# Optimization experiments

Measured on AMD Instinct MI355X. Metric: run time of the kernel, lower is better.

Reference implementation:

```python
import jax, jax.numpy as jnp
from jax import lax
import numpy as np

B, T = 128, 28
N = T - 1  # 27 recurrent steps


def conv(x, w, b, stride=1, pad=1):
    y = lax.conv_general_dilated(x, w, (stride, stride), [(pad, pad), (pad, pad)],
                                 dimension_numbers=('NCHW', 'OIHW', 'NCHW'))
    return y + b[None, :, None, None]


def convT(x, w, b, stride, pad, out_pad):
    # torch ConvTranspose2d: weight layout [in, out, k, k]
    k = w.shape[-1]
    wt = jnp.flip(w, (-2, -1)).transpose(1, 0, 2, 3)  # -> [out, in, k, k]
    lo, hi = k - 1 - pad, k - 1 - pad + out_pad
    y = lax.conv_general_dilated(x, wt, (1, 1), [(lo, hi), (lo, hi)],
                                 lhs_dilation=(stride, stride),
                                 dimension_numbers=('NCHW', 'OIHW', 'NCHW'))
    return y + b[None, :, None, None]


def setup_inputs():
    key = jax.random.key(0)
    ki = iter(jax.random.split(key, 48))
    def cw(o, i, k=3):
        return jax.random.normal(next(ki), (o, i, k, k), jnp.float32) / np.sqrt(i * k * k)
    def bias(o):
        return jax.random.normal(next(ki), (o,), jnp.float32) * 0.02
    H, I = 16 * 8 * 8, 48 * 8 * 8
    return {
        'x': jax.random.uniform(next(ki), (B, T, 3, 32, 32), jnp.float32),
        'eps': jax.random.normal(next(ki), (N, B, 64, 8, 8), jnp.float32),
        'psix1_w': cw(16, 3),  'psix1_b': bias(16),
        'psix2_w': cw(16, 16), 'psix2_b': bias(16),
        'psiz_w': cw(16, 64),  'psiz_b': bias(16),
        'enc1_w': cw(32, 32),  'enc1_b': bias(32),
        'enc2_w': cw(64, 32),  'enc2_b': bias(64),
        'encm_w': cw(64, 64),  'encm_b': bias(64),
        'encv_w': cw(64, 64),  'encv_b': bias(64),
        'pri_w': cw(32, 16),   'pri_b': bias(32),
        'prim_w': cw(64, 32),  'prim_b': bias(64),
        'priv_w': cw(64, 32),  'priv_b': bias(64),
        'dec1_w': jax.random.normal(next(ki), (32, 32, 3, 3), jnp.float32) / np.sqrt(32 * 9),
        'dec1_b': bias(32),
        'dec2_w': jax.random.normal(next(ki), (32, 3, 3, 3), jnp.float32) / np.sqrt(32 * 9),
        'dec2_b': bias(3),
        'gru_wi': jax.random.normal(next(ki), (3 * H, I), jnp.float32) / np.sqrt(I),
        'gru_wh': jax.random.normal(next(ki), (3 * H, H), jnp.float32) / np.sqrt(H),
        'gru_bi': bias(3 * H),
        'gru_bh': bias(3 * H),
    }


def _forward(x, eps, psix1_w, psix1_b, psix2_w, psix2_b, psiz_w, psiz_b,
             enc1_w, enc1_b, enc2_w, enc2_b, encm_w, encm_b, encv_w, encv_b,
             pri_w, pri_b, prim_w, prim_b, priv_w, priv_b,
             dec1_w, dec1_b, dec2_w, dec2_b, gru_wi, gru_wh, gru_bi, gru_bh):
    Bn = x.shape[0]
    Hf = 16 * 8 * 8
    n = x.shape[1] - 1

    def step(carry, inputs):
        h0, dec_prev, _, _, _, _ = carry
        frame, ep, idx = inputs
        cur = jnp.where(idx < 6, frame, dec_prev)
        px = jax.nn.relu(conv(cur, psix1_w, psix1_b, 2, 1))   # [B,16,16,16]
        px = jax.nn.relu(conv(px, psix2_w, psix2_b, 2, 1))    # [B,16,8,8]
        e = jnp.concatenate([px, h0], axis=1)                 # [B,32,8,8]
        e = jax.nn.relu(conv(e, enc1_w, enc1_b))
        e = jax.nn.relu(conv(e, enc2_w, enc2_b))              # [B,64,8,8]
        zm = conv(e, encm_w, encm_b)
        zlv = jax.nn.softplus(conv(e, encv_w, encv_b))
        p = jax.nn.relu(conv(h0, pri_w, pri_b))               # [B,32,8,8]
        pm = conv(p, prim_w, prim_b)
        plv = jax.nn.softplus(conv(p, priv_w, priv_b))
        z = zm + zlv * ep                                     # source's literal reparam (uses logvar, not std)
        zpsi = jax.nn.relu(conv(z, psiz_w, psiz_b))           # [B,16,8,8]
        d = jnp.concatenate([h0, zpsi], axis=1)               # [B,32,8,8]
        d = jax.nn.relu(convT(d, dec1_w, dec1_b, 2, 1, 0))    # 8 -> 15
        dec = jax.nn.sigmoid(convT(d, dec2_w, dec2_b, 2, 0, 1))  # 15 -> 32, [B,3,32,32]
        # GRUCell on flattened concat
        gi = jnp.concatenate([px, zpsi, h0], axis=1).reshape(Bn, -1)  # [B, 48*8*8]
        hf = h0.reshape(Bn, Hf)
        gih = gi @ gru_wi.T + gru_bi
        ghh = hf @ gru_wh.T + gru_bh
        ir, iz, inn = jnp.split(gih, 3, axis=1)
        hr, hz, hn = jnp.split(ghh, 3, axis=1)
        r = jax.nn.sigmoid(ir + hr)
        u = jax.nn.sigmoid(iz + hz)
        ng = jnp.tanh(inn + r * hn)
        hnew = ((1.0 - u) * ng + u * hf).reshape(Bn, 16, 8, 8)
        return (hnew, dec, zm, zlv, pm, plv), dec

    h0 = jnp.zeros((Bn, 16, 8, 8), jnp.float32)
    dec0 = jnp.zeros((Bn, 3, 32, 32), jnp.float32)
    s0 = jnp.zeros((Bn, 64, 8, 8), jnp.float32)
    frames = jnp.swapaxes(x[:, :n], 0, 1)  # [N,B,3,32,32]
    (_, _, zm, zlv, pm, plv), decs = lax.scan(
        step, (h0, dec0, s0, s0, s0, s0), (frames, eps, jnp.arange(n)))
    output = jnp.swapaxes(decs, 0, 1)  # [B,N,3,32,32]
    return output, zm, zlv, pm, plv


def reference(x, eps, psix1_w, psix1_b, psix2_w, psix2_b, psiz_w, psiz_b,
              enc1_w, enc1_b, enc2_w, enc2_b, encm_w, encm_b, encv_w, encv_b,
              pri_w, pri_b, prim_w, prim_b, priv_w, priv_b,
              dec1_w, dec1_b, dec2_w, dec2_b, gru_wi, gru_wh, gru_bi, gru_bh):
    return _forward(x, eps, psix1_w, psix1_b, psix2_w, psix2_b, psiz_w, psiz_b,
                    enc1_w, enc1_b, enc2_w, enc2_b, encm_w, encm_b, encv_w, encv_b,
                    pri_w, pri_b, prim_w, prim_b, priv_w, priv_b,
                    dec1_w, dec1_b, dec2_w, dec2_b, gru_wi, gru_wh, gru_bi, gru_bh)
```

## Files before the change

kernel.cpp:

```cpp
#include <hip/hip_runtime.h>

#define NSTEP 27

typedef _Float16 f16;
typedef __attribute__((ext_vector_type(8))) _Float16 f16x8;
typedef __attribute__((ext_vector_type(4))) float f32x4;

#define MFMA(a, b, c) __builtin_amdgcn_mfma_f32_16x16x32_f16(a, b, c, 0, 0, 0)

__device__ __forceinline__ float sigmoidf_(float x) { return 1.0f / (1.0f + expf(-x)); }
__device__ __forceinline__ float softplusf_(float x) { return x > 20.0f ? x : log1pf(expf(x)); }

constexpr long OFF_WI   = 0;
constexpr long OFF_WH   = OFF_WI   + 3072L * 3072;
constexpr long OFF_WPX1 = OFF_WH   + 3072L * 1024;
constexpr long OFF_WPX2 = OFF_WPX1 + 512;
constexpr long OFF_WE1  = OFF_WPX2 + 2560;
constexpr long OFF_WE2  = OFF_WE1  + 9216;
constexpr long OFF_WMV  = OFF_WE2  + 18432;
constexpr long OFF_WPZ  = OFF_WMV  + 73728;
constexpr long OFF_WPRI = OFF_WPZ  + 9216;
constexpr long OFF_WPMV = OFF_WPRI + 5120;
constexpr long OFF_WD1  = OFF_WPMV + 36864;
constexpr long OFF_GI   = OFF_WD1  + 9216;
constexpr long OFF_F16_END = OFF_GI + 128L * 3072;

struct Params {
  const float* frame; long fstride;
  const float* eps_t;
  const f16 *wpx1, *wpx2, *we1, *we2, *wmv, *wpz, *wd1, *wpri, *wpmv;
  const float *bpx1, *bpx2, *be1, *be2, *bm, *bv, *bpz, *bd1;
  const float *d2w, *d2b, *bpri, *bpm, *bpv, *gbi, *gbh;
  const float *gih0, *gih1, *ghh;
  float* hG; f16* gi;
  float *out_t, *zm, *zlv, *pm, *plv;
  int t, last;
};

__device__ __forceinline__ void scat8_lds(f16* __restrict__ A, int ldk, int pos, int ic, float val) {
  int py = pos >> 3, px = pos & 7;
  f16 v = (f16)val;
#pragma unroll
  for (int ky = 0; ky < 3; ++ky) {
    int oy = py + 1 - ky;
    if ((unsigned)oy >= 8u) continue;
#pragma unroll
    for (int kx = 0; kx < 3; ++kx) {
      int ox = px + 1 - kx;
      if ((unsigned)ox >= 8u) continue;
      A[(oy * 8 + ox) * ldk + ic * 9 + ky * 3 + kx] = v;
    }
  }
}

__device__ __forceinline__ void scatd1_lds(f16* __restrict__ Ad1, int pos, int ic, float val) {
  const int aof[4] = {0, 2560, 7168, 11776};
  const int Kp[4] = {40, 72, 72, 136};
  int py = pos >> 3, px = pos & 7;
  f16 v = (f16)val;
#pragma unroll
  for (int ky = 0; ky < 3; ++ky) {
    int y = 2 * py + ky - 1;
    if ((unsigned)y >= 15u) continue;
    int cy = y & 1;
    int nky = cy ? 2 : 1;
    int tiy = cy ? (ky >> 1) : 0;
#pragma unroll
    for (int kx = 0; kx < 3; ++kx) {
      int x = 2 * px + kx - 1;
      if ((unsigned)x >= 15u) continue;
      int cx = x & 1;
      int nkx = cx ? 2 : 1;
      int tix = cx ? (kx >> 1) : 0;
      int c = cy * 2 + cx;
      Ad1[aof[c] + ((y >> 1) * 8 + (x >> 1)) * Kp[c] + ic * (nky * nkx) + tiy * nkx + tix] = v;
    }
  }
}

__global__ __launch_bounds__(256) void k_wpack(const float* __restrict__ src, f16* __restrict__ dst,
                                               int N, int Ks, int Kd) {
  int tot = N * Kd, stride = gridDim.x * 256;
  for (int i = blockIdx.x * 256 + threadIdx.x; i < tot; i += stride) {
    int n = i / Kd, k = i - n * Kd;
    dst[i] = (k < Ks) ? (f16)src[n * Ks + k] : (f16)0.f;
  }
}

__global__ __launch_bounds__(256) void k_wd1(const float* __restrict__ src, f16* __restrict__ dst) {
  int i = blockIdx.x * 256 + threadIdx.x;
  if (i >= 9216) return;
  int c, base;
  if (i < 1024) { c = 0; base = 0; }
  else if (i < 3072) { c = 1; base = 1024; }
  else if (i < 5120) { c = 2; base = 3072; }
  else { c = 3; base = 5120; }
  const int Kc[4] = {32, 64, 64, 128};
  int j = i - base, K = Kc[c];
  int oc = j / K, k = j - oc * K;
  int cy = c >> 1, cx = c & 1;
  int nky = cy ? 2 : 1, nkx = cx ? 2 : 1, ntap = nky * nkx;
  int ic = k / ntap, tap = k - ic * ntap;
  int tiy = tap / nkx, tix = tap - tiy * nkx;
  int ky = (nky == 1) ? 1 : tiy * 2;
  int kx = (nkx == 1) ? 1 : tix * 2;
  dst[i] = (f16)src[((ic * 32 + oc) * 3 + ky) * 3 + kx];
}

__global__ __launch_bounds__(512) void k_step(Params P) {
  __shared__ f16 lds[78336];
  f16* hbuf = lds;
  f16* B1 = lds + 1024;
  f16* B2 = lds + 38400;
  f16* B3 = lds + 57344;
  f16* A1 = B3;
  f16* frame = B3 + 10240;
  f16* A2 = B3 + 10240;

  int b = blockIdx.x, tid = threadIdx.x;
  int wv = tid >> 6, lane = tid & 63, lm = lane & 15, q = lane >> 4;
  f32x4 z4 = {};

  for (int i = tid; i < 1024; i += 512) {
    float hn = 0.f;
    if (P.t) {
      long o = (long)b * 3072 + i;
      float ir  = P.gih0[o] + P.gih1[o] + P.gbi[i];
      float iz  = P.gih0[o + 1024] + P.gih1[o + 1024] + P.gbi[i + 1024];
      float in_ = P.gih0[o + 2048] + P.gih1[o + 2048] + P.gbi[i + 2048];
      float hr  = P.ghh[o] + P.gbh[i];
      float hz  = P.ghh[o + 1024] + P.gbh[i + 1024];
      float hnn = P.ghh[o + 2048] + P.gbh[i + 2048];
      float r = sigmoidf_(ir + hr), u = sigmoidf_(iz + hz);
      float ng = tanhf(in_ + r * hnn);
      hn = (1.f - u) * ng + u * P.hG[b * 1024 + i];
    }
    P.hG[b * 1024 + i] = hn;
    hbuf[i] = (f16)hn;
    P.gi[(long)b * 3072 + 2048 + i] = (f16)hn;
  }
  const float* fr = P.frame + (long)b * P.fstride;
  for (int i = tid; i < 3072; i += 512) frame[i] = (f16)fr[i];
  __syncthreads();
  {
    int row = tid >> 1, half = tid & 1;
    int oy = row >> 4, ox = row & 15;
    f16* rp = A1 + row * 40;
    if (half == 0) {
#pragma unroll
      for (int ic = 0; ic < 2; ++ic)
#pragma unroll
        for (int ky = 0; ky < 3; ++ky) {
          int y = 2 * oy + ky - 1;
#pragma unroll
          for (int kx = 0; kx < 3; ++kx) {
            int x = 2 * ox + kx - 1;
            rp[ic * 9 + ky * 3 + kx] =
                ((unsigned)y < 32u && (unsigned)x < 32u) ? frame[ic * 1024 + y * 32 + x] : (f16)0;
          }
        }
    } else {
#pragma unroll
      for (int ky = 0; ky < 3; ++ky) {
        int y = 2 * oy + ky - 1;
#pragma unroll
        for (int kx = 0; kx < 3; ++kx) {
          int x = 2 * ox + kx - 1;
          rp[18 + ky * 3 + kx] =
              ((unsigned)y < 32u && (unsigned)x < 32u) ? frame[2048 + y * 32 + x] : (f16)0;
        }
      }
#pragma unroll
      for (int k = 27; k < 40; ++k) rp[k] = (f16)0;
    }
  }
  __syncthreads();
  {
    int4 zz = {0, 0, 0, 0};
    for (int i = tid; i < 10752 / 8; i += 512) ((int4*)A2)[i] = zz;
    for (int i = tid; i < 18944 / 8; i += 512) ((int4*)B2)[i] = zz;
    for (int i = tid; i < 37376 / 8; i += 512) ((int4*)B1)[i] = zz;
  }
  __syncthreads();
  for (int i = tid; i < 1024; i += 512)
    scat8_lds(B2, 296, i & 63, 16 + (i >> 6), (float)hbuf[i]);
  {
    f16x8 bf = *(const f16x8*)(P.wpx1 + lm * 32 + q * 8);
    float bb = P.bpx1[lm];
#pragma unroll
    for (int mi = 0; mi < 2; ++mi) {
      int mt = wv * 2 + mi;
      f16x8 a = *(const f16x8*)(A1 + (mt * 16 + lm) * 40 + q * 8);
      f32x4 acc = MFMA(a, bf, z4);
#pragma unroll
      for (int r = 0; r < 4; ++r) {
        int m = mt * 16 + q * 4 + r;
        float val = fmaxf(acc[r] + bb, 0.f);
        int y = m >> 4, x = m & 15;
        f16 v = (f16)val;
#pragma unroll
        for (int ky = 0; ky < 3; ++ky) {
          int ty = y + 1 - ky;
          if (ty < 0 || (ty & 1)) continue;
          int oy = ty >> 1; if (oy >= 8) continue;
#pragma unroll
          for (int kx = 0; kx < 3; ++kx) {
            int tx = x + 1 - kx;
            if (tx < 0 || (tx & 1)) continue;
            int ox = tx >> 1; if (ox >= 8) continue;
            A2[(oy * 8 + ox) * 168 + lm * 9 + ky * 3 + kx] = v;
          }
        }
      }
    }
  }
  __syncthreads();
  if (wv < 4) {
    f32x4 acc = {};
#pragma unroll
    for (int k = 0; k < 160; k += 32) {
      f16x8 a = *(const f16x8*)(A2 + (wv * 16 + lm) * 168 + k + q * 8);
      f16x8 bf = *(const f16x8*)(P.wpx2 + lm * 160 + k + q * 8);
      acc = MFMA(a, bf, acc);
    }
    float bb = P.bpx2[lm];
#pragma unroll
    for (int r = 0; r < 4; ++r) {
      int pos = wv * 16 + q * 4 + r;
      float val = fmaxf(acc[r] + bb, 0.f);
      P.gi[(long)b * 3072 + lm * 64 + pos] = (f16)val;
      scat8_lds(B2, 296, pos, lm, val);
    }
  }
  __syncthreads();
  {
    int nt = wv & 1, mt = wv >> 1;
    f32x4 a0 = {};
#pragma unroll
    for (int k = 0; k < 288; k += 32) {
      f16x8 bf = *(const f16x8*)(P.we1 + (nt * 16 + lm) * 288 + k + q * 8);
      f16x8 x0 = *(const f16x8*)(B2 + (mt * 16 + lm) * 296 + k + q * 8);
      a0 = MFMA(x0, bf, a0);
    }
    for (int i = tid; i < 1024; i += 512)
      scatd1_lds(B3, i & 63, i >> 6, (float)hbuf[i]);
    __syncthreads();
    float bb = P.be1[nt * 16 + lm];
#pragma unroll
    for (int r = 0; r < 4; ++r)
      scat8_lds(B2, 296, mt * 16 + q * 4 + r, nt * 16 + lm, fmaxf(a0[r] + bb, 0.f));
  }
  __syncthreads();
  {
    int nt = wv & 3, mh = wv >> 2;
    f32x4 acc[2] = {};
#pragma unroll
    for (int k = 0; k < 288; k += 32) {
      f16x8 bf = *(const f16x8*)(P.we2 + (nt * 16 + lm) * 288 + k + q * 8);
#pragma unroll
      for (int mi = 0; mi < 2; ++mi) {
        f16x8 a = *(const f16x8*)(B2 + ((mh * 2 + mi) * 16 + lm) * 296 + k + q * 8);
        acc[mi] = MFMA(a, bf, acc[mi]);
      }
    }
    int ch = nt * 16 + lm;
    float bb = P.be2[ch];
#pragma unroll
    for (int mi = 0; mi < 2; ++mi)
#pragma unroll
      for (int r = 0; r < 4; ++r)
        scat8_lds(B1, 584, (mh * 2 + mi) * 16 + q * 4 + r, ch, fmaxf(acc[mi][r] + bb, 0.f));
  }
  __syncthreads();
  {
    f32x4 am[2] = {}, av[2] = {};
    int nq = wv & 3, mh = wv >> 2;
    int ch = nq * 16 + lm;
#pragma unroll 2
    for (int k = 0; k < 576; k += 32) {
      f16x8 bm = *(const f16x8*)(P.wmv + (long)ch * 576 + k + q * 8);
      f16x8 bv = *(const f16x8*)(P.wmv + (long)(64 + ch) * 576 + k + q * 8);
#pragma unroll
      for (int mi = 0; mi < 2; ++mi) {
        f16x8 a = *(const f16x8*)(B1 + ((mh * 2 + mi) * 16 + lm) * 584 + k + q * 8);
        am[mi] = MFMA(a, bm, am[mi]);
        av[mi] = MFMA(a, bv, av[mi]);
      }
    }
    __syncthreads();
    float bbm = P.bm[ch], bbv = P.bv[ch];
#pragma unroll
    for (int mi = 0; mi < 2; ++mi)
#pragma unroll
      for (int r = 0; r < 4; ++r) {
        int pos = (mh * 2 + mi) * 16 + q * 4 + r;
        float zmv = am[mi][r] + bbm;
        float sp = softplusf_(av[mi][r] + bbv);
        float zval = zmv + sp * P.eps_t[(long)b * 4096 + ch * 64 + pos];
        if (P.last) {
          P.zm[(long)b * 4096 + ch * 64 + pos] = zmv;
          P.zlv[(long)b * 4096 + ch * 64 + pos] = sp;
        }
        scat8_lds(B1, 584, pos, ch, zval);
      }
  }
  __syncthreads();
  if (wv < 4) {
    f32x4 acc = {};
#pragma unroll 2
    for (int k = 0; k < 576; k += 32) {
      f16x8 a = *(const f16x8*)(B1 + (wv * 16 + lm) * 584 + k + q * 8);
      f16x8 bf = *(const f16x8*)(P.wpz + (long)lm * 576 + k + q * 8);
      acc = MFMA(a, bf, acc);
    }
    float bb = P.bpz[lm];
#pragma unroll
    for (int r = 0; r < 4; ++r) {
      int pos = wv * 16 + q * 4 + r;
      float val = fmaxf(acc[r] + bb, 0.f);
      P.gi[(long)b * 3072 + 1024 + lm * 64 + pos] = (f16)val;
      scatd1_lds(B3, pos, 16 + lm, val);
    }
  }
  __syncthreads();
  {
    const int Kc[4] = {32, 64, 64, 128};
    const int Kp[4] = {40, 72, 72, 136};
    const int aof[4] = {0, 2560, 7168, 11776};
    const int bof[4] = {0, 1024, 3072, 5120};
    int nt = wv & 1, mt = wv >> 1;
#pragma unroll
    for (int c = 0; c < 4; ++c) {
      int cy = c >> 1, cx = c & 1;
      f32x4 acc = {};
      for (int k = 0; k < Kc[c]; k += 32) {
        f16x8 a = *(const f16x8*)(B3 + aof[c] + (mt * 16 + lm) * Kp[c] + k + q * 8);
        f16x8 bf = *(const f16x8*)(P.wd1 + bof[c] + (nt * 16 + lm) * Kc[c] + k + q * 8);
        acc = MFMA(a, bf, acc);
      }
      int oc = nt * 16 + lm;
      float bb = P.bd1[oc];
#pragma unroll
      for (int r = 0; r < 4; ++r) {
        int m = mt * 16 + q * 4 + r;
        int y = 2 * (m >> 3) + cy, x = 2 * (m & 7) + cx;
        if (y < 15 && x < 15)
          B2[oc * 240 + y * 15 + x] = (f16)fmaxf(acc[r] + bb, 0.f);
      }
    }
  }
  __syncthreads();
  {
    int p = wv & 3, jh = wv >> 2;
    int cy2 = p >> 1, cx2 = p & 1;
    int lx = lane & 15, ly = lane >> 4;
    int x = 2 * lx + cx2;
    float b0 = P.d2b[0], b1 = P.d2b[1], b2 = P.d2b[2];
    float acc[2][3];
#pragma unroll
    for (int j = 0; j < 2; ++j) { acc[j][0] = b0; acc[j][1] = b1; acc[j][2] = b2; }
    int nky = cy2 ? 1 : 2, nkx = cx2 ? 1 : 2;
    for (int ic = 0; ic < 32; ++ic) {
      const f16* sp = B2 + ic * 240;
      const float* wic = P.d2w + ic * 27;
      for (int ty = 0; ty < nky; ++ty) {
        int ky = cy2 ? 1 : ty * 2;
        for (int tx = 0; tx < nkx; ++tx) {
          int kx = cx2 ? 1 : tx * 2;
          int ix = (x - kx) >> 1;
          bool xv = (unsigned)ix < 15u;
          float w0 = wic[ky * 3 + kx];
          float w1 = wic[9 + ky * 3 + kx];
          float w2 = wic[18 + ky * 3 + kx];
#pragma unroll
          for (int j = 0; j < 2; ++j) {
            int py = (jh * 2 + j) * 4 + ly;
            int iy = (2 * py + cy2 - ky) >> 1;
            if (xv && (unsigned)iy < 15u) {
              float v = (float)sp[iy * 15 + ix];
              acc[j][0] += v * w0; acc[j][1] += v * w1; acc[j][2] += v * w2;
            }
          }
        }
      }
    }
#pragma unroll
    for (int j = 0; j < 2; ++j) {
      int y = 2 * ((jh * 2 + j) * 4 + ly) + cy2;
#pragma unroll
      for (int oc = 0; oc < 3; ++oc)
        P.out_t[(long)b * 82944 + oc * 1024 + y * 32 + x] = sigmoidf_(acc[j][oc]);
    }
  }
  if (P.last) {
    if (tid < 64) {
      int py = tid >> 3, px = tid & 7;
      f16* rp = B3 + tid * 168;
      int k = 0;
      for (int ic = 0; ic < 16; ++ic)
        for (int ky = 0; ky < 3; ++ky) {
          int y = py + ky - 1;
          for (int kx = 0; kx < 3; ++kx, ++k) {
            int x = px + kx - 1;
            rp[k] = ((unsigned)y < 8u && (unsigned)x < 8u) ? hbuf[ic * 64 + y * 8 + x] : (f16)0;
          }
        }
      for (; k < 168; ++k) rp[k] = (f16)0;
    }
    {
      int4 zz = {0, 0, 0, 0};
      for (int i = tid; i < 18944 / 8; i += 512) ((int4*)B1)[i] = zz;
    }
    __syncthreads();
    {
      int nt = wv & 1, mt = wv >> 1;
      f32x4 a0 = {};
#pragma unroll
      for (int k = 0; k < 160; k += 32) {
        f16x8 bf = *(const f16x8*)(P.wpri + (nt * 16 + lm) * 160 + k + q * 8);
        f16x8 x0 = *(const f16x8*)(B3 + (mt * 16 + lm) * 168 + k + q * 8);
        a0 = MFMA(x0, bf, a0);
      }
      float bb = P.bpri[nt * 16 + lm];
#pragma unroll
      for (int r = 0; r < 4; ++r)
        scat8_lds(B1, 296, mt * 16 + q * 4 + r, nt * 16 + lm, fmaxf(a0[r] + bb, 0.f));
    }
    __syncthreads();
    {
      f32x4 am[2] = {}, av[2] = {};
      int nq = wv & 3, mh = wv >> 2;
      int ch = nq * 16 + lm;
#pragma unroll
      for (int k = 0; k < 288; k += 32) {
        f16x8 bm = *(const f16x8*)(P.wpmv + (long)ch * 288 + k + q * 8);
        f16x8 bv = *(const f16x8*)(P.wpmv + (long)(64 + ch) * 288 + k + q * 8);
#pragma unroll
        for (int mi = 0; mi < 2; ++mi) {
          f16x8 a = *(const f16x8*)(B1 + ((mh * 2 + mi) * 16 + lm) * 296 + k + q * 8);
          am[mi] = MFMA(a, bm, am[mi]);
          av[mi] = MFMA(a, bv, av[mi]);
        }
      }
      float bbm = P.bpm[ch], bbv = P.bpv[ch];
#pragma unroll
      for (int mi = 0; mi < 2; ++mi)
#pragma unroll
        for (int r = 0; r < 4; ++r) {
          int pos = (mh * 2 + mi) * 16 + q * 4 + r;
          P.pm[(long)b * 4096 + ch * 64 + pos] = am[mi][r] + bbm;
          P.plv[(long)b * 4096 + ch * 64 + pos] = softplusf_(av[mi][r] + bbv);
        }
    }
  }
}

__global__ __launch_bounds__(128) void k_gru(const f16* __restrict__ gi,
                                             const f16* __restrict__ wi, const f16* __restrict__ wh,
                                             float* __restrict__ gih0, float* __restrict__ gih1,
                                             float* __restrict__ ghh) {
  int z = blockIdx.y;
  int wv = threadIdx.x >> 6, lane = threadIdx.x & 63, lm = lane & 15, q = lane >> 4;
  int gw = blockIdx.x * 2 + wv;
  int mg = gw & 1, ng = gw >> 1;
  const f16* A = (z == 2) ? gi + 2048 : gi;
  const f16* B = (z == 2) ? wh : wi;
  int K = (z == 2) ? 1024 : 1536;
  int k0 = (z == 1) ? 1536 : 0;
  long ldb = (z == 2) ? 1024 : 3072;
  float* out = (z == 0) ? gih0 : (z == 1) ? gih1 : ghh;
  int m0 = mg * 64, n0 = ng * 32;
  f32x4 acc[4][2] = {};
  const f16* Ap = A + (long)(m0 + lm) * 3072 + k0 + q * 8;
  const f16* Bp = B + (long)(n0 + lm) * ldb + k0 + q * 8;
#pragma unroll 2
  for (int k = 0; k < K; k += 32) {
    f16x8 b0 = *(const f16x8*)(Bp + k);
    f16x8 b1 = *(const f16x8*)(Bp + 16 * ldb + k);
#pragma unroll
    for (int i = 0; i < 4; ++i) {
      f16x8 a = *(const f16x8*)(Ap + (long)i * 16 * 3072 + k);
      acc[i][0] = MFMA(a, b0, acc[i][0]);
      acc[i][1] = MFMA(a, b1, acc[i][1]);
    }
  }
#pragma unroll
  for (int i = 0; i < 4; ++i)
#pragma unroll
    for (int j = 0; j < 2; ++j)
#pragma unroll
      for (int r = 0; r < 4; ++r)
        out[(long)(m0 + i * 16 + q * 4 + r) * 3072 + n0 + j * 16 + lm] = acc[i][j][r];
}

extern "C" void kernel_launch(void* const* d_in, const int* in_sizes, int n_in,
                              void* d_out, int out_size, void* d_ws, size_t ws_size,
                              hipStream_t stream) {
  const float* x       = (const float*)d_in[0];
  const float* eps     = (const float*)d_in[1];
  const float* psix1_w = (const float*)d_in[2];
  const float* psix1_b = (const float*)d_in[3];
  const float* psix2_w = (const float*)d_in[4];
  const float* psix2_b = (const float*)d_in[5];
  const float* psiz_w  = (const float*)d_in[6];
  const float* psiz_b  = (const float*)d_in[7];
  const float* enc1_w  = (const float*)d_in[8];
  const float* enc1_b  = (const float*)d_in[9];
  const float* enc2_w  = (const float*)d_in[10];
  const float* enc2_b  = (const float*)d_in[11];
  const float* encm_w  = (const float*)d_in[12];
  const float* encm_b  = (const float*)d_in[13];
  const float* encv_w  = (const float*)d_in[14];
  const float* encv_b  = (const float*)d_in[15];
  const float* pri_w   = (const float*)d_in[16];
  const float* pri_b   = (const float*)d_in[17];
  const float* prim_w  = (const float*)d_in[18];
  const float* prim_b  = (const float*)d_in[19];
  const float* priv_w  = (const float*)d_in[20];
  const float* priv_b  = (const float*)d_in[21];
  const float* dec1_w  = (const float*)d_in[22];
  const float* dec1_b  = (const float*)d_in[23];
  const float* dec2_w  = (const float*)d_in[24];
  const float* dec2_b  = (const float*)d_in[25];
  const float* gru_wi  = (const float*)d_in[26];
  const float* gru_wh  = (const float*)d_in[27];
  const float* gru_bi  = (const float*)d_in[28];
  const float* gru_bh  = (const float*)d_in[29];

  float* out = (float*)d_out;
  float* zm_out  = out + 10616832;
  float* zlv_out = zm_out + 524288;
  float* pm_out  = zlv_out + 524288;
  float* plv_out = pm_out + 524288;

  f16* ws16 = (f16*)d_ws;
  f16* wi_f  = ws16 + OFF_WI;
  f16* wh_f  = ws16 + OFF_WH;
  f16* w_px1 = ws16 + OFF_WPX1;
  f16* w_px2 = ws16 + OFF_WPX2;
  f16* w_e1  = ws16 + OFF_WE1;
  f16* w_e2  = ws16 + OFF_WE2;
  f16* w_mv  = ws16 + OFF_WMV;
  f16* w_pz  = ws16 + OFF_WPZ;
  f16* w_pri = ws16 + OFF_WPRI;
  f16* w_pmv = ws16 + OFF_WPMV;
  f16* w_d1  = ws16 + OFF_WD1;
  f16* gi    = ws16 + OFF_GI;
  float* fws = (float*)(ws16 + OFF_F16_END);
  float* gih0 = fws;
  float* gih1 = gih0 + 393216;
  float* ghh  = gih1 + 393216;
  float* hG   = ghh + 393216;

  k_wpack<<<2048, 256, 0, stream>>>(gru_wi, wi_f, 3072, 3072, 3072);
  k_wpack<<<1024, 256, 0, stream>>>(gru_wh, wh_f, 3072, 1024, 1024);
  k_wpack<<<2, 256, 0, stream>>>(psix1_w, w_px1, 16, 27, 32);
  k_wpack<<<10, 256, 0, stream>>>(psix2_w, w_px2, 16, 144, 160);
  k_wpack<<<36, 256, 0, stream>>>(enc1_w, w_e1, 32, 288, 288);
  k_wpack<<<72, 256, 0, stream>>>(enc2_w, w_e2, 64, 288, 288);
  k_wpack<<<144, 256, 0, stream>>>(encm_w, w_mv, 64, 576, 576);
  k_wpack<<<144, 256, 0, stream>>>(encv_w, w_mv + 64L * 576, 64, 576, 576);
  k_wpack<<<36, 256, 0, stream>>>(psiz_w, w_pz, 16, 576, 576);
  k_wpack<<<20, 256, 0, stream>>>(pri_w, w_pri, 32, 144, 160);
  k_wpack<<<72, 256, 0, stream>>>(prim_w, w_pmv, 64, 288, 288);
  k_wpack<<<72, 256, 0, stream>>>(priv_w, w_pmv + 64L * 288, 64, 288, 288);
  k_wd1<<<36, 256, 0, stream>>>(dec1_w, w_d1);

  for (int t = 0; t < NSTEP; ++t) {
    Params P;
    P.frame = (t < 6) ? x + (long)t * 3072 : out + (long)(t - 1) * 3072;
    P.fstride = (t < 6) ? 86016 : 82944;
    P.eps_t = eps + (long)t * 524288;
    P.wpx1 = w_px1; P.wpx2 = w_px2; P.we1 = w_e1; P.we2 = w_e2;
    P.wmv = w_mv; P.wpz = w_pz; P.wd1 = w_d1; P.wpri = w_pri; P.wpmv = w_pmv;
    P.bpx1 = psix1_b; P.bpx2 = psix2_b; P.be1 = enc1_b; P.be2 = enc2_b;
    P.bm = encm_b; P.bv = encv_b; P.bpz = psiz_b; P.bd1 = dec1_b;
    P.d2w = dec2_w; P.d2b = dec2_b; P.bpri = pri_b; P.bpm = prim_b; P.bpv = priv_b;
    P.gbi = gru_bi; P.gbh = gru_bh;
    P.gih0 = gih0; P.gih1 = gih1; P.ghh = ghh;
    P.hG = hG; P.gi = gi;
    P.out_t = out + (long)t * 3072;
    P.zm = zm_out; P.zlv = zlv_out; P.pm = pm_out; P.plv = plv_out;
    P.t = t; P.last = (t == NSTEP - 1);
    k_step<<<128, 512, 0, stream>>>(P);
    if (t < NSTEP - 1)
      k_gru<<<dim3(96, 3), 128, 0, stream>>>(gi, wi_f, wh_f, gih0, gih1, ghh);
  }
}
```

Before: 2.736 ms.

## Double k_step block to 1024 threads and split per-wave work across 16 waves

Launches the per-sample step kernel with 1024 threads instead of 512 and redistributes each conv stage so every wave handles one M tile instead of two. The zeroing of LDS buffers is overlapped with im2col construction, and the transposed-conv decoder phases are split across more waves. This targets latency in a kernel with only 128 blocks by exposing more parallelism per block. The cost is higher register pressure under the 1024-thread launch bound and idle waves in stages that only use 4 or 8 waves.

```diff
diff --git a/kernel.cpp b/kernel.cpp
--- a/kernel.cpp
+++ b/kernel.cpp
@@ -107,7 +107,7 @@
   dst[i] = (f16)src[((ic * 32 + oc) * 3 + ky) * 3 + kx];
 }
 
-__global__ __launch_bounds__(512) void k_step(Params P) {
+__global__ __launch_bounds__(1024) void k_step(Params P) {
   __shared__ f16 lds[78336];
   f16* hbuf = lds;
   f16* B1 = lds + 1024;
@@ -121,7 +121,8 @@
   int wv = tid >> 6, lane = tid & 63, lm = lane & 15, q = lane >> 4;
   f32x4 z4 = {};
 
-  for (int i = tid; i < 1024; i += 512) {
+  {
+    int i = tid;
     float hn = 0.f;
     if (P.t) {
       long o = (long)b * 3072 + i;
@@ -140,9 +141,9 @@
     P.gi[(long)b * 3072 + 2048 + i] = (f16)hn;
   }
   const float* fr = P.frame + (long)b * P.fstride;
-  for (int i = tid; i < 3072; i += 512) frame[i] = (f16)fr[i];
-  __syncthreads();
-  {
+  for (int i = tid; i < 3072; i += 1024) frame[i] = (f16)fr[i];
+  __syncthreads();
+  if (tid < 512) {
     int row = tid >> 1, half = tid & 1;
     int oy = row >> 4, ox = row & 15;
     f16* rp = A1 + row * 40;
@@ -173,43 +174,42 @@
 #pragma unroll
       for (int k = 27; k < 40; ++k) rp[k] = (f16)0;
     }
-  }
-  __syncthreads();
-  {
+  } else {
     int4 zz = {0, 0, 0, 0};
-    for (int i = tid; i < 10752 / 8; i += 512) ((int4*)A2)[i] = zz;
-    for (int i = tid; i < 18944 / 8; i += 512) ((int4*)B2)[i] = zz;
-    for (int i = tid; i < 37376 / 8; i += 512) ((int4*)B1)[i] = zz;
-  }
-  __syncthreads();
-  for (int i = tid; i < 1024; i += 512)
-    scat8_lds(B2, 296, i & 63, 16 + (i >> 6), (float)hbuf[i]);
+    int t2 = tid - 512;
+    for (int i = t2; i < 18944 / 8; i += 512) ((int4*)B2)[i] = zz;
+    for (int i = t2; i < 37376 / 8; i += 512) ((int4*)B1)[i] = zz;
+  }
+  __syncthreads();
+  {
+    int4 zz = {0, 0, 0, 0};
+    for (int i = tid; i < 10752 / 8; i += 1024) ((int4*)A2)[i] = zz;
+  }
+  __syncthreads();
+  scat8_lds(B2, 296, tid & 63, 16 + (tid >> 6), (float)hbuf[tid]);
   {
     f16x8 bf = *(const f16x8*)(P.wpx1 + lm * 32 + q * 8);
     float bb = P.bpx1[lm];
-#pragma unroll
-    for (int mi = 0; mi < 2; ++mi) {
-      int mt = wv * 2 + mi;
-      f16x8 a = *(const f16x8*)(A1 + (mt * 16 + lm) * 40 + q * 8);
-      f32x4 acc = MFMA(a, bf, z4);
-#pragma unroll
-      for (int r = 0; r < 4; ++r) {
-        int m = mt * 16 + q * 4 + r;
-        float val = fmaxf(acc[r] + bb, 0.f);
-        int y = m >> 4, x = m & 15;
-        f16 v = (f16)val;
-#pragma unroll
-        for (int ky = 0; ky < 3; ++ky) {
-          int ty = y + 1 - ky;
-          if (ty < 0 || (ty & 1)) continue;
-          int oy = ty >> 1; if (oy >= 8) continue;
-#pragma unroll
-          for (int kx = 0; kx < 3; ++kx) {
-            int tx = x + 1 - kx;
-            if (tx < 0 || (tx & 1)) continue;
-            int ox = tx >> 1; if (ox >= 8) continue;
-            A2[(oy * 8 + ox) * 168 + lm * 9 + ky * 3 + kx] = v;
-          }
+    int mt = wv;
+    f16x8 a = *(const f16x8*)(A1 + (mt * 16 + lm) * 40 + q * 8);
+    f32x4 acc = MFMA(a, bf, z4);
+#pragma unroll
+    for (int r = 0; r < 4; ++r) {
+      int m = mt * 16 + q * 4 + r;
+      float val = fmaxf(acc[r] + bb, 0.f);
+      int y = m >> 4, x = m & 15;
+      f16 v = (f16)val;
+#pragma unroll
+      for (int ky = 0; ky < 3; ++ky) {
+        int ty = y + 1 - ky;
+        if (ty < 0 || (ty & 1)) continue;
+        int oy = ty >> 1; if (oy >= 8) continue;
+#pragma unroll
+        for (int kx = 0; kx < 3; ++kx) {
+          int tx = x + 1 - kx;
+          if (tx < 0 || (tx & 1)) continue;
+          int ox = tx >> 1; if (ox >= 8) continue;
+          A2[(oy * 8 + ox) * 168 + lm * 9 + ky * 3 + kx] = v;
         }
       }
     }
@@ -234,80 +234,77 @@
   }
   __syncthreads();
   {
-    int nt = wv & 1, mt = wv >> 1;
+    int nt = wv & 1, mt = (wv >> 1) & 3;
     f32x4 a0 = {};
-#pragma unroll
-    for (int k = 0; k < 288; k += 32) {
-      f16x8 bf = *(const f16x8*)(P.we1 + (nt * 16 + lm) * 288 + k + q * 8);
-      f16x8 x0 = *(const f16x8*)(B2 + (mt * 16 + lm) * 296 + k + q * 8);
-      a0 = MFMA(x0, bf, a0);
-    }
-    for (int i = tid; i < 1024; i += 512)
-      scatd1_lds(B3, i & 63, i >> 6, (float)hbuf[i]);
+    if (wv < 8) {
+#pragma unroll
+      for (int k = 0; k < 288; k += 32) {
+        f16x8 bf = *(const f16x8*)(P.we1 + (nt * 16 + lm) * 288 + k + q * 8);
+        f16x8 x0 = *(const f16x8*)(B2 + (mt * 16 + lm) * 296 + k + q * 8);
+        a0 = MFMA(x0, bf, a0);
+      }
+    } else {
+      int i0 = (wv - 8) * 128 + lane;
+      scatd1_lds(B3, i0 & 63, i0 >> 6, (float)hbuf[i0]);
+      int i1 = i0 + 64;
+      scatd1_lds(B3, i1 & 63, i1 >> 6, (float)hbuf[i1]);
+    }
     __syncthreads();
-    float bb = P.be1[nt * 16 + lm];
-#pragma unroll
-    for (int r = 0; r < 4; ++r)
-      scat8_lds(B2, 296, mt * 16 + q * 4 + r, nt * 16 + lm, fmaxf(a0[r] + bb, 0.f));
+    if (wv < 8) {
+      float bb = P.be1[nt * 16 + lm];
+#pragma unroll
+      for (int r = 0; r < 4; ++r)
+        scat8_lds(B2, 296, mt * 16 + q * 4 + r, nt * 16 + lm, fmaxf(a0[r] + bb, 0.f));
+    }
   }
   __syncthreads();
   {
     int nt = wv & 3, mh = wv >> 2;
-    f32x4 acc[2] = {};
+    f32x4 acc = {};
 #pragma unroll
     for (int k = 0; k < 288; k += 32) {
       f16x8 bf = *(const f16x8*)(P.we2 + (nt * 16 + lm) * 288 + k + q * 8);
-#pragma unroll
-      for (int mi = 0; mi < 2; ++mi) {
-        f16x8 a = *(const f16x8*)(B2 + ((mh * 2 + mi) * 16 + lm) * 296 + k + q * 8);
-        acc[mi] = MFMA(a, bf, acc[mi]);
-      }
+      f16x8 a = *(const f16x8*)(B2 + ((mh)*16 + lm) * 296 + k + q * 8);
+      acc = MFMA(a, bf, acc);
     }
     int ch = nt * 16 + lm;
     float bb = P.be2[ch];
 #pragma unroll
-    for (int mi = 0; mi < 2; ++mi)
-#pragma unroll
-      for (int r = 0; r < 4; ++r)
-        scat8_lds(B1, 584, (mh * 2 + mi) * 16 + q * 4 + r, ch, fmaxf(acc[mi][r] + bb, 0.f));
-  }
-  __syncthreads();
-  {
-    f32x4 am[2] = {}, av[2] = {};
+    for (int r = 0; r < 4; ++r)
+      scat8_lds(B1, 584, mh * 16 + q * 4 + r, ch, fmaxf(acc[r] + bb, 0.f));
+  }
+  __syncthreads();
+  {
+    f32x4 am = {}, av = {};
     int nq = wv & 3, mh = wv >> 2;
     int ch = nq * 16 + lm;
-#pragma unroll 2
+#pragma unroll
     for (int k = 0; k < 576; k += 32) {
       f16x8 bm = *(const f16x8*)(P.wmv + (long)ch * 576 + k + q * 8);
       f16x8 bv = *(const f16x8*)(P.wmv + (long)(64 + ch) * 576 + k + q * 8);
-#pragma unroll
-      for (int mi = 0; mi < 2; ++mi) {
-        f16x8 a = *(const f16x8*)(B1 + ((mh * 2 + mi) * 16 + lm) * 584 + k + q * 8);
-        am[mi] = MFMA(a, bm, am[mi]);
-        av[mi] = MFMA(a, bv, av[mi]);
-      }
+      f16x8 a = *(const f16x8*)(B1 + (mh * 16 + lm) * 584 + k + q * 8);
+      am = MFMA(a, bm, am);
+      av = MFMA(a, bv, av);
     }
     __syncthreads();
     float bbm = P.bm[ch], bbv = P.bv[ch];
 #pragma unroll
-    for (int mi = 0; mi < 2; ++mi)
-#pragma unroll
-      for (int r = 0; r < 4; ++r) {
-        int pos = (mh * 2 + mi) * 16 + q * 4 + r;
-        float zmv = am[mi][r] + bbm;
-        float sp = softplusf_(av[mi][r] + bbv);
-        float zval = zmv + sp * P.eps_t[(long)b * 4096 + ch * 64 + pos];
-        if (P.last) {
-          P.zm[(long)b * 4096 + ch * 64 + pos] = zmv;
-          P.zlv[(long)b * 4096 + ch * 64 + pos] = sp;
-        }
-        scat8_lds(B1, 584, pos, ch, zval);
-      }
+    for (int r = 0; r < 4; ++r) {
+      int pos = mh * 16 + q * 4 + r;
+      float zmv = am[r] + bbm;
+      float sp = softplusf_(av[r] + bbv);
+      float zval = zmv + sp * P.eps_t[(long)b * 4096 + ch * 64 + pos];
+      if (P.last) {
+        P.zm[(long)b * 4096 + ch * 64 + pos] = zmv;
+        P.zlv[(long)b * 4096 + ch * 64 + pos] = sp;
+      }
+      scat8_lds(B1, 584, pos, ch, zval);
+    }
   }
   __syncthreads();
   if (wv < 4) {
     f32x4 acc = {};
-#pragma unroll 2
+#pragma unroll
     for (int k = 0; k < 576; k += 32) {
       f16x8 a = *(const f16x8*)(B1 + (wv * 16 + lm) * 584 + k + q * 8);
       f16x8 bf = *(const f16x8*)(P.wpz + (long)lm * 576 + k + q * 8);
@@ -324,18 +321,19 @@
   }
   __syncthreads();
   {
-    const int Kc[4] = {32, 64, 64, 128};
-    const int Kp[4] = {40, 72, 72, 136};
-    const int aof[4] = {0, 2560, 7168, 11776};
-    const int bof[4] = {0, 1024, 3072, 5120};
-    int nt = wv & 1, mt = wv >> 1;
-#pragma unroll
-    for (int c = 0; c < 4; ++c) {
+    int nt = wv & 1, mt = (wv >> 1) & 3, cb = wv >> 3;
+#pragma unroll
+    for (int cc = 0; cc < 2; ++cc) {
+      int c = cb + cc * 2;
       int cy = c >> 1, cx = c & 1;
+      int Kc = 32 << (cy + cx);
+      int Kp = Kc + 8;
+      int aof = cy ? (cx ? 11776 : 7168) : (cx ? 2560 : 0);
+      int bof = cy ? (cx ? 5120 : 3072) : (cx ? 1024 : 0);
       f32x4 acc = {};
-      for (int k = 0; k < Kc[c]; k += 32) {
-        f16x8 a = *(const f16x8*)(B3 + aof[c] + (mt * 16 + lm) * Kp[c] + k + q * 8);
-        f16x8 bf = *(const f16x8*)(P.wd1 + bof[c] + (nt * 16 + lm) * Kc[c] + k + q * 8);
+      for (int k = 0; k < Kc; k += 32) {
+        f16x8 a = *(const f16x8*)(B3 + aof + (mt * 16 + lm) * Kp + k + q * 8);
+        f16x8 bf = *(const f16x8*)(P.wd1 + bof + (nt * 16 + lm) * Kc + k + q * 8);
         acc = MFMA(a, bf, acc);
       }
       int oc = nt * 16 + lm;
@@ -355,42 +353,32 @@
     int cy2 = p >> 1, cx2 = p & 1;
     int lx = lane & 15, ly = lane >> 4;
     int x = 2 * lx + cx2;
-    float b0 = P.d2b[0], b1 = P.d2b[1], b2 = P.d2b[2];
-    float acc[2][3];
-#pragma unroll
-    for (int j = 0; j < 2; ++j) { acc[j][0] = b0; acc[j][1] = b1; acc[j][2] = b2; }
+    float acc0 = P.d2b[0], acc1 = P.d2b[1], acc2 = P.d2b[2];
     int nky = cy2 ? 1 : 2, nkx = cx2 ? 1 : 2;
+    int py = jh * 4 + ly;
     for (int ic = 0; ic < 32; ++ic) {
       const f16* sp = B2 + ic * 240;
       const float* wic = P.d2w + ic * 27;
       for (int ty = 0; ty < nky; ++ty) {
         int ky = cy2 ? 1 : ty * 2;
+        int iy = (2 * py + cy2 - ky) >> 1;
+        bool yv = (unsigned)iy < 15u;
         for (int tx = 0; tx < nkx; ++tx) {
           int kx = cx2 ? 1 : tx * 2;
           int ix = (x - kx) >> 1;
-          bool xv = (unsigned)ix < 15u;
-          float w0 = wic[ky * 3 + kx];
-          float w1 = wic[9 + ky * 3 + kx];
-          float w2 = wic[18 + ky * 3 + kx];
-#pragma unroll
-          for (int j = 0; j < 2; ++j) {
-            int py = (jh * 2 + j) * 4 + ly;
-            int iy = (2 * py + cy2 - ky) >> 1;
-            if (xv && (unsigned)iy < 15u) {
-              float v = (float)sp[iy * 15 + ix];
-              acc[j][0] += v * w0; acc[j][1] += v * w1; acc[j][2] += v * w2;
-            }
+          if (yv && (unsigned)ix < 15u) {
+            float v = (float)sp[iy * 15 + ix];
+            acc0 += v * wic[ky * 3 + kx];
+            acc1 += v * wic[9 + ky * 3 + kx];
+            acc2 += v * wic[18 + ky * 3 + kx];
           }
         }
       }
     }
-#pragma unroll
-    for (int j = 0; j < 2; ++j) {
-      int y = 2 * ((jh * 2 + j) * 4 + ly) + cy2;
-#pragma unroll
-      for (int oc = 0; oc < 3; ++oc)
-        P.out_t[(long)b * 82944 + oc * 1024 + y * 32 + x] = sigmoidf_(acc[j][oc]);
-    }
+    int y = 2 * py + cy2;
+    P.out_t[(long)b * 82944 + 0 * 1024 + y * 32 + x] = sigmoidf_(acc0);
+    P.out_t[(long)b * 82944 + 1 * 1024 + y * 32 + x] = sigmoidf_(acc1);
+    P.out_t[(long)b * 82944 + 2 * 1024 + y * 32 + x] = sigmoidf_(acc2);
   }
   if (P.last) {
     if (tid < 64) {
@@ -409,10 +397,10 @@
     }
     {
       int4 zz = {0, 0, 0, 0};
-      for (int i = tid; i < 18944 / 8; i += 512) ((int4*)B1)[i] = zz;
+      for (int i = tid; i < 18944 / 8; i += 1024) ((int4*)B1)[i] = zz;
     }
     __syncthreads();
-    {
+    if (wv < 8) {
       int nt = wv & 1, mt = wv >> 1;
       f32x4 a0 = {};
 #pragma unroll
@@ -428,29 +416,24 @@
     }
     __syncthreads();
     {
-      f32x4 am[2] = {}, av[2] = {};
+      f32x4 am = {}, av = {};
       int nq = wv & 3, mh = wv >> 2;
       int ch = nq * 16 + lm;
 #pragma unroll
       for (int k = 0; k < 288; k += 32) {
         f16x8 bm = *(const f16x8*)(P.wpmv + (long)ch * 288 + k + q * 8);
         f16x8 bv = *(const f16x8*)(P.wpmv + (long)(64 + ch) * 288 + k + q * 8);
-#pragma unroll
-        for (int mi = 0; mi < 2; ++mi) {
-          f16x8 a = *(const f16x8*)(B1 + ((mh * 2 + mi) * 16 + lm) * 296 + k + q * 8);
-          am[mi] = MFMA(a, bm, am[mi]);
-          av[mi] = MFMA(a, bv, av[mi]);
-        }
+        f16x8 a = *(const f16x8*)(B1 + (mh * 16 + lm) * 296 + k + q * 8);
+        am = MFMA(a, bm, am);
+        av = MFMA(a, bv, av);
       }
       float bbm = P.bpm[ch], bbv = P.bpv[ch];
 #pragma unroll
-      for (int mi = 0; mi < 2; ++mi)
-#pragma unroll
-        for (int r = 0; r < 4; ++r) {
-          int pos = (mh * 2 + mi) * 16 + q * 4 + r;
-          P.pm[(long)b * 4096 + ch * 64 + pos] = am[mi][r] + bbm;
-          P.plv[(long)b * 4096 + ch * 64 + pos] = softplusf_(av[mi][r] + bbv);
-        }
+      for (int r = 0; r < 4; ++r) {
+        int pos = mh * 16 + q * 4 + r;
+        P.pm[(long)b * 4096 + ch * 64 + pos] = am[r] + bbm;
+        P.plv[(long)b * 4096 + ch * 64 + pos] = softplusf_(av[r] + bbv);
+      }
     }
   }
 }
@@ -582,7 +565,7 @@
     P.out_t = out + (long)t * 3072;
     P.zm = zm_out; P.zlv = zlv_out; P.pm = pm_out; P.plv = plv_out;
     P.t = t; P.last = (t == NSTEP - 1);
-    k_step<<<128, 512, 0, stream>>>(P);
+    k_step<<<128, 1024, 0, stream>>>(P);
     if (t < NSTEP - 1)
       k_gru<<<dim3(96, 3), 128, 0, stream>>>(gi, wi_f, wh_f, gih0, gih1, ghh);
   }
```

After: 2.710 ms. About the same (-1.0%).
